# Optimization experiments

Measured on AMD Instinct MI355X. Metric: run time of the kernel, lower is better.

The kernel has to match this reference:

```python
import jax, jax.numpy as jnp
import numpy as np

N = 4096
E = 131072
IN_C, HID, HEADS, OUT_C = 512, 64, 8, 256
BETA = 0.5
NEG_SLOPE = 0.2


def _glorot(key, shape, fan_in, fan_out):
    lim = float(np.sqrt(6.0 / (fan_in + fan_out)))
    return jax.random.uniform(key, shape, jnp.float32, -lim, lim)


def setup_inputs() -> dict:
    key = jax.random.key(0)
    ks = jax.random.split(key, 12)
    x = jax.random.normal(ks[0], (N, IN_C), jnp.float32)
    src = jax.random.randint(ks[1], (E,), 0, N)
    dst = jax.random.randint(ks[2], (E,), 0, N)
    dst = jnp.where(src == dst, (dst + 1) % N, dst)  # no self loops (module removes then re-adds)
    edge_index = jnp.stack([src, dst]).astype(jnp.int64)
    # layer 1: in=512 -> heads=8, out=64 (concat -> 512), residual=False
    W1 = _glorot(ks[3], (IN_C, HEADS * HID), IN_C, HEADS * HID)
    as1 = _glorot(ks[4], (HEADS, HID), HID, HID)
    ad1 = _glorot(ks[5], (HEADS, HID), HID, HID)
    b1 = jnp.zeros((HEADS * HID,), jnp.float32)
    # layer 2: in=512 -> heads=1, out=256, concat=False, residual=True (res_linear needed)
    W2 = _glorot(ks[6], (HEADS * HID, OUT_C), HEADS * HID, OUT_C)
    as2 = _glorot(ks[7], (1, OUT_C), OUT_C, OUT_C)
    ad2 = _glorot(ks[8], (1, OUT_C), OUT_C, OUT_C)
    b2 = jnp.zeros((OUT_C,), jnp.float32)
    resW2 = _glorot(ks[9], (HEADS * HID, OUT_C), HEADS * HID, OUT_C)
    return {"x": x, "edge_index": edge_index, "W1": W1, "as1": as1, "ad1": ad1,
            "b1": b1, "W2": W2, "as2": as2, "ad2": ad2, "b2": b2, "resW2": resW2}


def _seg_softmax(e, seg, n):
    # numerically-stable softmax over edges grouped by destination node
    m = jax.ops.segment_max(e, seg, num_segments=n)  # [n, H]
    a = jnp.exp(e - m[seg])
    s = jax.ops.segment_sum(a, seg, num_segments=n)
    return a / (s[seg] + 1e-16)


def _motif_gat_layer(x, edge_index, W, a_src, a_dst, bias, res_W, heads, out_ch, concat):
    n = x.shape[0]
    residual = x
    h = (x @ W).reshape(n, heads, out_ch)
    # add self loops (input edge_index has none)
    loops = jnp.arange(n, dtype=edge_index.dtype)
    src = jnp.concatenate([edge_index[0], loops])
    dst = jnp.concatenate([edge_index[1], loops])
    xj = h[src]  # [E', H, C]
    xi = h[dst]
    e = (xj * a_src[None]).sum(-1) + (xi * a_dst[None]).sum(-1)  # [E', H]
    alpha_first = _seg_softmax(jax.nn.leaky_relu(e, NEG_SLOPE), dst, n)
    # motif adjacency: dense A^3, row-normalized by clamped row sum
    adj = jnp.zeros((n, n), x.dtype).at[src, dst].set(1.0)
    m3 = adj @ adj @ adj
    m3 = m3 / jnp.clip(m3.sum(-1, keepdims=True), 1.0)
    mw = m3[src, dst][:, None]  # [E', 1]
    alpha_motif = _seg_softmax(jax.nn.leaky_relu(e * mw, NEG_SLOPE), dst, n)
    alpha = BETA * alpha_first + (1.0 - BETA) * alpha_motif  # dropout: eval mode -> identity
    out = jax.ops.segment_sum(alpha[:, :, None] * xj, dst, num_segments=n)  # [n, H, C]
    out = out.reshape(n, heads * out_ch) if concat else out.mean(1)
    if res_W is not None:
        out = out + residual @ res_W
    return out + bias


def reference(x, edge_index, W1, as1, ad1, b1, W2, as2, ad2, b2, resW2):
    h = _motif_gat_layer(x, edge_index, W1, as1, ad1, b1, None, HEADS, HID, True)
    h = jax.nn.elu(h)  # dropout: eval mode -> identity
    out = _motif_gat_layer(h, edge_index, W2, as2, ad2, b2, resW2, 1, OUT_C, False)
    return out
```

## Files before the change

kernel.cpp:

```cpp
#include <hip/hip_runtime.h>
#include <hip/hip_bf16.h>
#include <math.h>

#define NN 4096
#define EE 131072
#define EP (EE + NN)
#define C1 512
#define H1 8
#define C2 256
#define NWORDS 128
#define KP 520

typedef __attribute__((ext_vector_type(8))) short bf16x8;
typedef __attribute__((ext_vector_type(4))) float f32x4;

__device__ __forceinline__ float wredMaxf(float v){
#pragma unroll
  for(int o=32;o;o>>=1) v = fmaxf(v, __shfl_xor(v,o));
  return v;
}
__device__ __forceinline__ float wredSumf(float v){
#pragma unroll
  for(int o=32;o;o>>=1) v += __shfl_xor(v,o);
  return v;
}
__device__ __forceinline__ int wredSumi(int v){
#pragma unroll
  for(int o=32;o;o>>=1) v += __shfl_xor(v,o);
  return v;
}

__device__ __forceinline__ void bfsplit(float v, unsigned short& h, unsigned short& l){
  unsigned bits = __float_as_uint(v);
  h = (unsigned short)(bits>>16);
  float hf = __uint_as_float(bits & 0xFFFF0000u);
  float lo = v - hf;
  l = (unsigned short)(__float_as_uint(lo)>>16);
}

__global__ __launch_bounds__(256) void k_detect(const int* __restrict__ ei32, int* __restrict__ mode){
  __shared__ int any;
  if(threadIdx.x==0) any = 0;
  __syncthreads();
  int nz = 0;
  for(int i=threadIdx.x;i<2048;i+=256) nz |= (ei32[2*i+1] != 0);
  if(nz) atomicOr(&any, 1);
  __syncthreads();
  if(threadIdx.x==0) *mode = any;
}

__device__ __forceinline__ void edge_sd(const int* ei32, int mode, int e, int& s, int& d){
  if(e < EE){
    if(mode==0){ s = ei32[2*e]; d = ei32[2*(EE+e)]; }
    else       { s = ei32[e];   d = ei32[EE+e]; }
  } else { s = e - EE; d = s; }
}

__global__ __launch_bounds__(256) void k_build(const int* __restrict__ ei32, const int* __restrict__ mode,
    unsigned* __restrict__ rowbits, unsigned* __restrict__ colbits, unsigned* __restrict__ cnt){
  int e = blockIdx.x*256 + threadIdx.x;
  if(e >= EP) return;
  int m = *mode, s, d;
  edge_sd(ei32, m, e, s, d);
  atomicOr(&rowbits[s*NWORDS + (d>>5)], 1u<<(d&31));
  atomicOr(&colbits[d*NWORDS + (s>>5)], 1u<<(s&31));
  atomicAdd(&cnt[d], 1u);
}

__global__ __launch_bounds__(256) void k_scan(const unsigned* __restrict__ cnt, unsigned* __restrict__ rowptr){
  __shared__ unsigned part[256];
  int t = threadIdx.x;
  unsigned loc[16]; unsigned s = 0;
#pragma unroll
  for(int i=0;i<16;i++){ loc[i]=cnt[t*16+i]; s+=loc[i]; }
  part[t]=s; __syncthreads();
  for(int off=1;off<256;off<<=1){
    unsigned v = (t>=off)? part[t-off] : 0u;
    __syncthreads();
    part[t]+=v;
    __syncthreads();
  }
  unsigned run = (t==0)? 0u : part[t-1];
#pragma unroll
  for(int i=0;i<16;i++){ rowptr[t*16+i]=run; run+=loc[i]; }
  if(t==255) rowptr[NN]=run;
}

__global__ __launch_bounds__(256) void k_fill(const int* __restrict__ ei32, const int* __restrict__ mode,
    const unsigned* __restrict__ rowptr, unsigned* __restrict__ fill,
    unsigned* __restrict__ csr_src){
  int e = blockIdx.x*256 + threadIdx.x;
  if(e >= EP) return;
  int m = *mode, s, d;
  edge_sd(ei32, m, e, s, d);
  unsigned pos = rowptr[d] + atomicAdd(&fill[d], 1u);
  csr_src[pos]=(unsigned)s;
}

__global__ __launch_bounds__(256) void k_deg(const unsigned* __restrict__ rowbits, float* __restrict__ v1){
  int node = blockIdx.x*4 + (threadIdx.x>>6);
  int lane = threadIdx.x & 63;
  unsigned w0 = rowbits[node*NWORDS + 2*lane];
  unsigned w1 = rowbits[node*NWORDS + 2*lane + 1];
  int c = __popc(w0) + __popc(w1);
  c = wredSumi(c);
  if(lane==0) v1[node] = (float)c;
}

__global__ __launch_bounds__(256) void k_mv(const unsigned* __restrict__ rowbits,
    const float* __restrict__ vin, float* __restrict__ vout){
  int node = blockIdx.x*4 + (threadIdx.x>>6);
  int lane = threadIdx.x & 63;
  float sum = 0.f;
  unsigned w = rowbits[node*NWORDS + 2*lane]; int b0 = lane*64;
  while(w){ int b=__ffs(w)-1; sum += vin[b0+b]; w &= w-1; }
  w = rowbits[node*NWORDS + 2*lane + 1]; b0 = lane*64 + 32;
  while(w){ int b=__ffs(w)-1; sum += vin[b0+b]; w &= w-1; }
  sum = wredSumf(sum);
  if(lane==0) vout[node] = sum;
}

__global__ __launch_bounds__(64) void k_motif(const unsigned* __restrict__ rowbits, const unsigned* __restrict__ colbits,
    const unsigned* __restrict__ rowptr, const unsigned* __restrict__ csr_src,
    const float* __restrict__ v3, float* __restrict__ mwc){
  int d = blockIdx.x;
  int lane = threadIdx.x;
  __shared__ unsigned short nbr[1024];
  __shared__ int cntL;
  if(lane==0) cntL=0;
  __syncthreads();
  {
    unsigned w = colbits[d*NWORDS + 2*lane]; int b0 = lane*64;
    while(w){ int b=__ffs(w)-1; int pos=atomicAdd(&cntL,1); nbr[pos]=(unsigned short)(b0+b); w&=w-1; }
    w = colbits[d*NWORDS + 2*lane + 1]; b0 = lane*64 + 32;
    while(w){ int b=__ffs(w)-1; int pos=atomicAdd(&cntL,1); nbr[pos]=(unsigned short)(b0+b); w&=w-1; }
  }
  __syncthreads();
  int m = cntL;
  unsigned gp[8][2];
#pragma unroll
  for(int p=0;p<8;p++){ gp[p][0]=0u; gp[p][1]=0u; }
  for(int t0=0;t0<m;t0+=4){
    unsigned xa[4], xb[4];
#pragma unroll
    for(int j=0;j<4;j++){
      int tt=t0+j;
      if(tt<m){ int l = nbr[tt]; xa[j]=colbits[l*NWORDS+2*lane]; xb[j]=colbits[l*NWORDS+2*lane+1]; }
      else    { xa[j]=0u; xb[j]=0u; }
    }
#pragma unroll
    for(int j=0;j<4;j++){
      unsigned c = xa[j];
#pragma unroll
      for(int p=0;p<8;p++){ unsigned cy = gp[p][0] & c; gp[p][0] ^= c; c = cy; }
      c = xb[j];
#pragma unroll
      for(int p=0;p<8;p++){ unsigned cy = gp[p][1] & c; gp[p][1] ^= c; c = cy; }
    }
  }
  unsigned base = rowptr[d], deg = rowptr[d+1]-base;
  for(unsigned i0=0;i0<deg;i0+=4){
    unsigned sidx[4], ra[4], rb[4];
#pragma unroll
    for(int j=0;j<4;j++){
      unsigned ii = (i0+j < deg) ? (i0+j) : (deg-1);
      sidx[j] = csr_src[base+ii];
    }
#pragma unroll
    for(int j=0;j<4;j++){ ra[j]=rowbits[sidx[j]*NWORDS+2*lane]; rb[j]=rowbits[sidx[j]*NWORDS+2*lane+1]; }
    int sum[4];
#pragma unroll
    for(int j=0;j<4;j++){
      int s=0;
#pragma unroll
      for(int p=0;p<8;p++)
        s += (__popc(ra[j]&gp[p][0]) + __popc(rb[j]&gp[p][1])) << p;
      sum[j]=s;
    }
    int pk0 = sum[0] | (sum[1]<<16);
    int pk1 = sum[2] | (sum[3]<<16);
    pk0 = wredSumi(pk0); pk1 = wredSumi(pk1);
    if(lane==0){
      int ss[4] = { pk0 & 0xFFFF, (pk0>>16)&0xFFFF, pk1 & 0xFFFF, (pk1>>16)&0xFFFF };
#pragma unroll
      for(int j=0;j<4;j++){
        unsigned idx = i0+j;
        if(idx<deg)
          mwc[base+idx] = (float)ss[j] / fmaxf(v3[csr_src[base+idx]], 1.0f);
      }
    }
  }
}

__global__ __launch_bounds__(256) void k_cvtA(const float* __restrict__ X,
    unsigned short* __restrict__ xh, unsigned short* __restrict__ xl){
  int e = blockIdx.x*256 + threadIdx.x;
  int row = e >> 6;
  int c0 = (e & 63) * 8;
  const float4 v0 = *(const float4*)&X[(size_t)row*C1 + c0];
  const float4 v1 = *(const float4*)&X[(size_t)row*C1 + c0 + 4];
  float vv[8] = {v0.x,v0.y,v0.z,v0.w,v1.x,v1.y,v1.z,v1.w};
  unsigned short h[8], l[8];
#pragma unroll
  for(int j=0;j<8;j++) bfsplit(vv[j], h[j], l[j]);
  *(bf16x8*)&xh[(size_t)row*KP + c0] = *(bf16x8*)h;
  *(bf16x8*)&xl[(size_t)row*KP + c0] = *(bf16x8*)l;
}

__global__ __launch_bounds__(256) void k_cvtB(const float* __restrict__ W, int N,
    unsigned short* __restrict__ bh, unsigned short* __restrict__ bl){
  int n = blockIdx.x; int t = threadIdx.x;
  int k = t*2;
  float a = W[(size_t)k*N + n];
  float b = W[(size_t)(k+1)*N + n];
  unsigned short h0,l0,h1,l1;
  bfsplit(a,h0,l0); bfsplit(b,h1,l1);
  unsigned short hp[2]={h0,h1}, lp[2]={l0,l1};
  *(unsigned int*)&bh[(size_t)n*KP + k] = *(unsigned int*)hp;
  *(unsigned int*)&bl[(size_t)n*KP + k] = *(unsigned int*)lp;
}

__global__ __launch_bounds__(256) void k_gemm_mfma(
    const unsigned short* __restrict__ Ah, const unsigned short* __restrict__ Al,
    const unsigned short* __restrict__ Bh, const unsigned short* __restrict__ Bl,
    float* __restrict__ C, int M, int N){
  __shared__ unsigned short Ahs[64][40], Als[64][40], Bhs[64][40], Bls[64][40];
  int bm = blockIdx.y*64, bn = blockIdx.x*64;
  int t = threadIdx.x, lane = t&63, w = t>>6;
  int wm = (w>>1)*32, wn = (w&1)*32;
  f32x4 acc[2][2];
#pragma unroll
  for(int i=0;i<2;i++)
#pragma unroll
    for(int j=0;j<2;j++) acc[i][j] = (f32x4){0.f,0.f,0.f,0.f};
  int sm = t>>2, skq = (t&3)*8;
  const unsigned short* pAh = &Ah[(size_t)(bm+sm)*KP + skq];
  const unsigned short* pAl = &Al[(size_t)(bm+sm)*KP + skq];
  const unsigned short* pBh = &Bh[(size_t)(bn+sm)*KP + skq];
  const unsigned short* pBl = &Bl[(size_t)(bn+sm)*KP + skq];
  int fr = lane&15, kg = lane>>4;
  for(int k0=0;k0<C1;k0+=32){
    *(bf16x8*)&Ahs[sm][skq] = *(const bf16x8*)(pAh + k0);
    *(bf16x8*)&Als[sm][skq] = *(const bf16x8*)(pAl + k0);
    *(bf16x8*)&Bhs[sm][skq] = *(const bf16x8*)(pBh + k0);
    *(bf16x8*)&Bls[sm][skq] = *(const bf16x8*)(pBl + k0);
    __syncthreads();
    bf16x8 ah[2], al[2], bh[2], bl[2];
#pragma unroll
    for(int i=0;i<2;i++){
      ah[i] = *(bf16x8*)&Ahs[wm + i*16 + fr][kg*8];
      al[i] = *(bf16x8*)&Als[wm + i*16 + fr][kg*8];
      bh[i] = *(bf16x8*)&Bhs[wn + i*16 + fr][kg*8];
      bl[i] = *(bf16x8*)&Bls[wn + i*16 + fr][kg*8];
    }
#pragma unroll
    for(int i=0;i<2;i++)
#pragma unroll
      for(int j=0;j<2;j++){
        acc[i][j] = __builtin_amdgcn_mfma_f32_16x16x32_bf16(ah[i], bh[j], acc[i][j], 0,0,0);
        acc[i][j] = __builtin_amdgcn_mfma_f32_16x16x32_bf16(ah[i], bl[j], acc[i][j], 0,0,0);
        acc[i][j] = __builtin_amdgcn_mfma_f32_16x16x32_bf16(al[i], bh[j], acc[i][j], 0,0,0);
      }
    __syncthreads();
  }
#pragma unroll
  for(int i=0;i<2;i++)
#pragma unroll
    for(int j=0;j<2;j++){
      int gr = bm + wm + i*16 + kg*4;
      int gc = bn + wn + j*16 + fr;
#pragma unroll
      for(int e=0;e<4;e++)
        C[(size_t)(gr+e)*N + gc] = acc[i][j][e];
    }
}

__global__ __launch_bounds__(512) void k_attn1(const float* __restrict__ hpre, const float* __restrict__ as1,
    const float* __restrict__ ad1, float* __restrict__ asrc, float* __restrict__ adst){
  int n = blockIdx.x; int t = threadIdx.x; int lane = t&63; int h = t>>6;
  float v = hpre[n*C1 + t];
  float p1 = v*as1[t], p2 = v*ad1[t];
  p1 = wredSumf(p1); p2 = wredSumf(p2);
  if(lane==0){ asrc[n*H1+h]=p1; adst[n*H1+h]=p2; }
}

__global__ __launch_bounds__(128) void k_layer1(const unsigned* __restrict__ rowptr, const unsigned* __restrict__ csr_src,
    const float* __restrict__ mwc, const float* __restrict__ asrc, const float* __restrict__ adst,
    const float* __restrict__ hpre, const float* __restrict__ b1,
    unsigned short* __restrict__ h1h, unsigned short* __restrict__ h1l){
  int n = blockIdx.x;
  int tid = threadIdx.x, lane = tid&63, wv = tid>>6;
  unsigned base = rowptr[n], deg = rowptr[n+1]-base;
  __shared__ float a1s[128][9];
  __shared__ float a2s[128][9];
  __shared__ unsigned ssrc[128];
  __shared__ float red1[2][8], red2[2][8];
  __shared__ float snm1[8], snm2[8], sscl1[8], sscl2[8];
  __shared__ float sS1[8], sS2[8], sM1[8], sM2[8];
  __shared__ float adsts[8];
  if(tid<8){ adsts[tid]=adst[n*H1+tid]; sM1[tid]=-3.0e38f; sM2[tid]=-3.0e38f; sS1[tid]=0.f; sS2[tid]=0.f; }
  __syncthreads();
  int h = tid>>4;
  float4 acc1={0.f,0.f,0.f,0.f}, acc2={0.f,0.f,0.f,0.f};
  for(unsigned c0=0;c0<deg;c0+=128){
    int csz = (int)min(128u, deg-c0);
    bool act = (tid < csz);
    float el[8], em[8];
    if(act){
      unsigned s = csr_src[base+c0+tid];
      ssrc[tid]=s;
      float mwv = mwc[base+c0+tid];
      const float4 a0v = *(const float4*)&asrc[s*H1];
      const float4 a1v = *(const float4*)&asrc[s*H1+4];
      float as8[8]={a0v.x,a0v.y,a0v.z,a0v.w,a1v.x,a1v.y,a1v.z,a1v.w};
#pragma unroll
      for(int hh=0;hh<8;hh++){
        float ev = as8[hh]+adsts[hh];
        el[hh] = ev>=0.f? ev : 0.2f*ev;
        float evm = ev*mwv;
        em[hh] = evm>=0.f? evm : 0.2f*evm;
      }
    } else {
#pragma unroll
      for(int hh=0;hh<8;hh++){ el[hh]=-3.0e38f; em[hh]=-3.0e38f; }
    }
    float mx1[8], mx2[8];
#pragma unroll
    for(int hh=0;hh<8;hh++){ mx1[hh]=wredMaxf(el[hh]); mx2[hh]=wredMaxf(em[hh]); }
    if(lane==0){
#pragma unroll
      for(int hh=0;hh<8;hh++){ red1[wv][hh]=mx1[hh]; red2[wv][hh]=mx2[hh]; }
    }
    __syncthreads();
    if(tid<8){
      float cm1 = fmaxf(red1[0][tid], red1[1][tid]);
      float cm2 = fmaxf(red2[0][tid], red2[1][tid]);
      float nm1 = fmaxf(sM1[tid], cm1), nm2 = fmaxf(sM2[tid], cm2);
      sscl1[tid] = expf(sM1[tid]-nm1); sscl2[tid] = expf(sM2[tid]-nm2);
      snm1[tid]=nm1; snm2[tid]=nm2;
      sM1[tid]=nm1;  sM2[tid]=nm2;
    }
    __syncthreads();
    float s1l[8], s2l[8];
#pragma unroll
    for(int hh=0;hh<8;hh++){
      float a1v = act? expf(el[hh]-snm1[hh]) : 0.f;
      float a2v = act? expf(em[hh]-snm2[hh]) : 0.f;
      if(act){ a1s[tid][hh]=a1v; a2s[tid][hh]=a2v; }
      s1l[hh]=a1v; s2l[hh]=a2v;
    }
#pragma unroll
    for(int hh=0;hh<8;hh++){ s1l[hh]=wredSumf(s1l[hh]); s2l[hh]=wredSumf(s2l[hh]); }
    if(lane==0){
#pragma unroll
      for(int hh=0;hh<8;hh++){ red1[wv][hh]=s1l[hh]; red2[wv][hh]=s2l[hh]; }
    }
    __syncthreads();
    if(tid<8){
      sS1[tid] = sS1[tid]*sscl1[tid] + red1[0][tid]+red1[1][tid];
      sS2[tid] = sS2[tid]*sscl2[tid] + red2[0][tid]+red2[1][tid];
    }
    {
      float sc1 = sscl1[h], sc2 = sscl2[h];
      acc1.x*=sc1; acc1.y*=sc1; acc1.z*=sc1; acc1.w*=sc1;
      acc2.x*=sc2; acc2.y*=sc2; acc2.z*=sc2; acc2.w*=sc2;
    }
    for(int i0=0;i0<csz;i0+=4){
      int jn = min(4, csz-i0);
      unsigned sj[4]; float a1j[4], a2j[4];
#pragma unroll
      for(int j=0;j<4;j++){
        int ii = (j<jn)? i0+j : i0;
        sj[j]=ssrc[ii]; a1j[j]=a1s[ii][h]; a2j[j]=a2s[ii][h];
      }
      float4 hv[4];
#pragma unroll
      for(int j=0;j<4;j++) hv[j] = *(const float4*)&hpre[(size_t)sj[j]*C1 + tid*4];
#pragma unroll
      for(int j=0;j<4;j++){
        float w1 = (j<jn)? a1j[j] : 0.f;
        float w2 = (j<jn)? a2j[j] : 0.f;
        acc1.x += w1*hv[j].x; acc1.y += w1*hv[j].y; acc1.z += w1*hv[j].z; acc1.w += w1*hv[j].w;
        acc2.x += w2*hv[j].x; acc2.y += w2*hv[j].y; acc2.z += w2*hv[j].z; acc2.w += w2*hv[j].w;
      }
    }
    __syncthreads();
  }
  float r1 = 0.5f/(sS1[h]+1e-16f), r2 = 0.5f/(sS2[h]+1e-16f);
  int cc = tid*4;
  const float4 bv = *(const float4*)&b1[cc];
  float o[4];
  float vx = acc1.x*r1 + acc2.x*r2 + bv.x; o[0] = vx>0.f? vx : expm1f(vx);
  float vy = acc1.y*r1 + acc2.y*r2 + bv.y; o[1] = vy>0.f? vy : expm1f(vy);
  float vz = acc1.z*r1 + acc2.z*r2 + bv.z; o[2] = vz>0.f? vz : expm1f(vz);
  float vw = acc1.w*r1 + acc2.w*r2 + bv.w; o[3] = vw>0.f? vw : expm1f(vw);
  unsigned short hh4[4], ll4[4];
#pragma unroll
  for(int j=0;j<4;j++) bfsplit(o[j], hh4[j], ll4[j]);
  *(ushort4*)&h1h[(size_t)n*KP + cc] = *(ushort4*)hh4;
  *(ushort4*)&h1l[(size_t)n*KP + cc] = *(ushort4*)ll4;
}

__global__ __launch_bounds__(64) void k_attn2(const float* __restrict__ h2, const float* __restrict__ as2,
    const float* __restrict__ ad2, float* __restrict__ asrc, float* __restrict__ adst){
  int n = blockIdx.x; int lane = threadIdx.x;
  const float4 hv = *(const float4*)&h2[(size_t)n*512 + lane*4];
  const float4 av = *(const float4*)&as2[lane*4];
  const float4 dv = *(const float4*)&ad2[lane*4];
  float p1 = hv.x*av.x + hv.y*av.y + hv.z*av.z + hv.w*av.w;
  float p2 = hv.x*dv.x + hv.y*dv.y + hv.z*dv.z + hv.w*dv.w;
  p1 = wredSumf(p1); p2 = wredSumf(p2);
  if(lane==0){ asrc[n]=p1; adst[n]=p2; }
}

__global__ __launch_bounds__(64) void k_layer2(const unsigned* __restrict__ rowptr, const unsigned* __restrict__ csr_src,
    const float* __restrict__ mwc, const float* __restrict__ asrc, const float* __restrict__ adst,
    const float* __restrict__ h2, const float* __restrict__ res,
    const float* __restrict__ b2, float* __restrict__ out){
  int n = blockIdx.x; int lane = threadIdx.x;
  unsigned base = rowptr[n], deg = rowptr[n+1]-base;
  __shared__ float a1s[64], a2s[64];
  __shared__ unsigned ssrc[64];
  float ad = adst[n];
  float M1=-3.0e38f, M2=-3.0e38f, S1=0.f, S2=0.f;
  float4 acc1={0.f,0.f,0.f,0.f}, acc2={0.f,0.f,0.f,0.f};
  for(unsigned c0=0;c0<deg;c0+=64){
    int csz = (int)min(64u, deg-c0);
    bool act = (lane < csz);
    float el=-3.0e38f, em=-3.0e38f;
    if(act){
      unsigned s = csr_src[base+c0+lane];
      ssrc[lane]=s;
      float mwv = mwc[base+c0+lane];
      float ev = asrc[s] + ad;
      el = ev>=0.f? ev : 0.2f*ev;
      float evm = ev*mwv;
      em = evm>=0.f? evm : 0.2f*evm;
    }
    float nm1 = fmaxf(M1, wredMaxf(el));
    float nm2 = fmaxf(M2, wredMaxf(em));
    float sc1 = expf(M1-nm1), sc2 = expf(M2-nm2);
    M1=nm1; M2=nm2;
    float a1 = act? expf(el-nm1) : 0.f;
    float a2 = act? expf(em-nm2) : 0.f;
    if(act){ a1s[lane]=a1; a2s[lane]=a2; }
    S1 = S1*sc1 + wredSumf(a1);
    S2 = S2*sc2 + wredSumf(a2);
    acc1.x*=sc1; acc1.y*=sc1; acc1.z*=sc1; acc1.w*=sc1;
    acc2.x*=sc2; acc2.y*=sc2; acc2.z*=sc2; acc2.w*=sc2;
    __syncthreads();
    for(int i0=0;i0<csz;i0+=4){
      int jn = min(4, csz-i0);
      unsigned sj[4]; float a1j[4], a2j[4];
#pragma unroll
      for(int j=0;j<4;j++){
        int ii = (j<jn)? i0+j : i0;
        sj[j]=ssrc[ii]; a1j[j]=a1s[ii]; a2j[j]=a2s[ii];
      }
      float4 hv[4];
#pragma unroll
      for(int j=0;j<4;j++) hv[j] = *(const float4*)&h2[(size_t)sj[j]*512 + lane*4];
#pragma unroll
      for(int j=0;j<4;j++){
        float w1 = (j<jn)? a1j[j] : 0.f;
        float w2 = (j<jn)? a2j[j] : 0.f;
        acc1.x += w1*hv[j].x; acc1.y += w1*hv[j].y; acc1.z += w1*hv[j].z; acc1.w += w1*hv[j].w;
        acc2.x += w2*hv[j].x; acc2.y += w2*hv[j].y; acc2.z += w2*hv[j].z; acc2.w += w2*hv[j].w;
      }
    }
    __syncthreads();
  }
  float r1 = 0.5f/(S1+1e-16f), r2 = 0.5f/(S2+1e-16f);
  int cc = lane*4;
  const float4 rv = *(const float4*)&res[(size_t)n*512 + cc];
  const float4 bv = *(const float4*)&b2[cc];
  float4 o = {acc1.x*r1 + acc2.x*r2 + rv.x + bv.x,
              acc1.y*r1 + acc2.y*r2 + rv.y + bv.y,
              acc1.z*r1 + acc2.z*r2 + rv.z + bv.z,
              acc1.w*r1 + acc2.w*r2 + rv.w + bv.w};
  *(float4*)&out[(size_t)n*C2 + cc] = o;
}

extern "C" void kernel_launch(void* const* d_in, const int* in_sizes, int n_in,
                              void* d_out, int out_size, void* d_ws, size_t ws_size,
                              hipStream_t stream) {
  const float* x    = (const float*)d_in[0];
  const int*   ei32 = (const int*)d_in[1];
  const float* W1   = (const float*)d_in[2];
  const float* as1  = (const float*)d_in[3];
  const float* ad1  = (const float*)d_in[4];
  const float* b1   = (const float*)d_in[5];
  const float* W2   = (const float*)d_in[6];
  const float* as2  = (const float*)d_in[7];
  const float* ad2  = (const float*)d_in[8];
  const float* b2   = (const float*)d_in[9];
  const float* resW2= (const float*)d_in[10];
  float* out = (float*)d_out;

  char* p = (char*)d_ws;
  auto alloc = [&](size_t b){ void* r=(void*)p; p += (b + 255) & ~(size_t)255; return r; };
  unsigned* rowbits = (unsigned*)alloc((size_t)NN*NWORDS*4);
  unsigned* colbits = (unsigned*)alloc((size_t)NN*NWORDS*4);
  unsigned* cnt     = (unsigned*)alloc(NN*4);
  unsigned* fill    = (unsigned*)alloc(NN*4);
  unsigned* rowptr  = (unsigned*)alloc((NN+4)*4);
  float* v1 = (float*)alloc(NN*4);
  float* v2 = (float*)alloc(NN*4);
  float* v3 = (float*)alloc(NN*4);
  unsigned* csr_src = (unsigned*)alloc((size_t)EP*4);
  float* mwc  = (float*)alloc((size_t)EP*4);
  float* asrc1= (float*)alloc(NN*H1*4);
  float* adst1= (float*)alloc(NN*H1*4);
  unsigned short* xsh = (unsigned short*)alloc((size_t)NN*KP*2);
  unsigned short* xsl = (unsigned short*)alloc((size_t)NN*KP*2);
  unsigned short* bt1h= (unsigned short*)alloc((size_t)C1*KP*2);
  unsigned short* bt1l= (unsigned short*)alloc((size_t)C1*KP*2);
  unsigned short* bt2h= (unsigned short*)alloc((size_t)C1*KP*2);
  unsigned short* bt2l= (unsigned short*)alloc((size_t)C1*KP*2);
  float* hpre = (float*)alloc((size_t)NN*C1*4);
  unsigned short* h1h = (unsigned short*)alloc((size_t)NN*KP*2);
  unsigned short* h1l = (unsigned short*)alloc((size_t)NN*KP*2);
  float* c23  = (float*)alloc((size_t)NN*512*4);
  float* asrc2= (float*)alloc(NN*4);
  float* adst2= (float*)alloc(NN*4);
  int* mode   = (int*)alloc(256);
  float* h2  = c23;
  float* res = c23 + 256;

  hipMemsetAsync(rowbits, 0, (size_t)NN*NWORDS*4*2, stream);
  hipMemsetAsync(cnt, 0, (size_t)NN*4*2, stream);

  k_detect<<<1,256,0,stream>>>(ei32, mode);
  k_build<<<(EP+255)/256,256,0,stream>>>(ei32, mode, rowbits, colbits, cnt);
  k_scan<<<1,256,0,stream>>>(cnt, rowptr);
  k_fill<<<(EP+255)/256,256,0,stream>>>(ei32, mode, rowptr, fill, csr_src);
  k_deg<<<NN/4,256,0,stream>>>(rowbits, v1);
  k_mv<<<NN/4,256,0,stream>>>(rowbits, v1, v2);
  k_mv<<<NN/4,256,0,stream>>>(rowbits, v2, v3);
  k_motif<<<NN,64,0,stream>>>(rowbits, colbits, rowptr, csr_src, v3, mwc);

  k_cvtA<<<(NN*64)/256,256,0,stream>>>(x, xsh, xsl);
  k_cvtB<<<C1,256,0,stream>>>(W1, C1, bt1h, bt1l);
  k_cvtB<<<C2,256,0,stream>>>(W2, C2, bt2h, bt2l);
  k_cvtB<<<C2,256,0,stream>>>(resW2, C2, bt2h + (size_t)C2*KP, bt2l + (size_t)C2*KP);

  k_gemm_mfma<<<dim3(C1/64, NN/64),256,0,stream>>>(xsh, xsl, bt1h, bt1l, hpre, NN, C1);
  k_attn1<<<NN,512,0,stream>>>(hpre, as1, ad1, asrc1, adst1);
  k_layer1<<<NN,128,0,stream>>>(rowptr, csr_src, mwc, asrc1, adst1, hpre, b1, h1h, h1l);

  k_gemm_mfma<<<dim3(512/64, NN/64),256,0,stream>>>(h1h, h1l, bt2h, bt2l, c23, NN, 512);
  k_attn2<<<NN,64,0,stream>>>(h2, as2, ad2, asrc2, adst2);
  k_layer2<<<NN,64,0,stream>>>(rowptr, csr_src, mwc, asrc2, adst2, h2, res, b2, out);
}
```

Baseline: 267.7 us.

## Fold mode detection into build kernels, merge launches, pipeline GEMM, widen gathers

Drops the separate mode-detection kernel and has each edge kernel infer int32/int64 layout from the first few words. The two memsets become one, and the three weight-conversion launches become one kernel, cutting launch count. The MFMA GEMM now uses a K tile of 64 with register prefetch of the next tile, so global loads overlap compute, and the layer aggregation loops gather 8 neighbour rows per batch instead of 4. The detection heuristic samples only 8 words and could misclassify unusual inputs, and the larger batches raise register pressure.

```diff
diff --git a/kernel.cpp b/kernel.cpp
--- a/kernel.cpp
+++ b/kernel.cpp
@@ -38,15 +38,11 @@
   l = (unsigned short)(__float_as_uint(lo)>>16);
 }
 
-__global__ __launch_bounds__(256) void k_detect(const int* __restrict__ ei32, int* __restrict__ mode){
-  __shared__ int any;
-  if(threadIdx.x==0) any = 0;
-  __syncthreads();
-  int nz = 0;
-  for(int i=threadIdx.x;i<2048;i+=256) nz |= (ei32[2*i+1] != 0);
-  if(nz) atomicOr(&any, 1);
-  __syncthreads();
-  if(threadIdx.x==0) *mode = any;
+__device__ __forceinline__ int detect_mode(const int* __restrict__ ei32){
+  unsigned nz = 0;
+#pragma unroll
+  for(int i=1;i<16;i+=2) nz |= (unsigned)ei32[i];
+  return nz != 0;
 }
 
 __device__ __forceinline__ void edge_sd(const int* ei32, int mode, int e, int& s, int& d){
@@ -56,11 +52,11 @@
   } else { s = e - EE; d = s; }
 }
 
-__global__ __launch_bounds__(256) void k_build(const int* __restrict__ ei32, const int* __restrict__ mode,
+__global__ __launch_bounds__(256) void k_build(const int* __restrict__ ei32,
     unsigned* __restrict__ rowbits, unsigned* __restrict__ colbits, unsigned* __restrict__ cnt){
   int e = blockIdx.x*256 + threadIdx.x;
   if(e >= EP) return;
-  int m = *mode, s, d;
+  int m = detect_mode(ei32), s, d;
   edge_sd(ei32, m, e, s, d);
   atomicOr(&rowbits[s*NWORDS + (d>>5)], 1u<<(d&31));
   atomicOr(&colbits[d*NWORDS + (s>>5)], 1u<<(s&31));
@@ -86,12 +82,12 @@
   if(t==255) rowptr[NN]=run;
 }
 
-__global__ __launch_bounds__(256) void k_fill(const int* __restrict__ ei32, const int* __restrict__ mode,
+__global__ __launch_bounds__(256) void k_fill(const int* __restrict__ ei32,
     const unsigned* __restrict__ rowptr, unsigned* __restrict__ fill,
     unsigned* __restrict__ csr_src){
   int e = blockIdx.x*256 + threadIdx.x;
   if(e >= EP) return;
-  int m = *mode, s, d;
+  int m = detect_mode(ei32), s, d;
   edge_sd(ei32, m, e, s, d);
   unsigned pos = rowptr[d] + atomicAdd(&fill[d], 1u);
   csr_src[pos]=(unsigned)s;
@@ -207,24 +203,30 @@
   *(bf16x8*)&xl[(size_t)row*KP + c0] = *(bf16x8*)l;
 }
 
-__global__ __launch_bounds__(256) void k_cvtB(const float* __restrict__ W, int N,
-    unsigned short* __restrict__ bh, unsigned short* __restrict__ bl){
-  int n = blockIdx.x; int t = threadIdx.x;
+__global__ __launch_bounds__(256) void k_cvtB_all(const float* __restrict__ W1f,
+    const float* __restrict__ W2f, const float* __restrict__ Wrf,
+    unsigned short* __restrict__ b1h, unsigned short* __restrict__ b1l,
+    unsigned short* __restrict__ b2h, unsigned short* __restrict__ b2l){
+  int blk = blockIdx.x; int t = threadIdx.x;
+  const float* W; int N, n, nrow; unsigned short *bh, *bl;
+  if(blk < 512){ W=W1f; N=512; n=blk;     nrow=n;     bh=b1h; bl=b1l; }
+  else if(blk < 768){ W=W2f; N=256; n=blk-512; nrow=n;     bh=b2h; bl=b2l; }
+  else { W=Wrf; N=256; n=blk-768; nrow=n+256; bh=b2h; bl=b2l; }
   int k = t*2;
   float a = W[(size_t)k*N + n];
   float b = W[(size_t)(k+1)*N + n];
   unsigned short h0,l0,h1,l1;
   bfsplit(a,h0,l0); bfsplit(b,h1,l1);
   unsigned short hp[2]={h0,h1}, lp[2]={l0,l1};
-  *(unsigned int*)&bh[(size_t)n*KP + k] = *(unsigned int*)hp;
-  *(unsigned int*)&bl[(size_t)n*KP + k] = *(unsigned int*)lp;
+  *(unsigned int*)&bh[(size_t)nrow*KP + k] = *(unsigned int*)hp;
+  *(unsigned int*)&bl[(size_t)nrow*KP + k] = *(unsigned int*)lp;
 }
 
 __global__ __launch_bounds__(256) void k_gemm_mfma(
     const unsigned short* __restrict__ Ah, const unsigned short* __restrict__ Al,
     const unsigned short* __restrict__ Bh, const unsigned short* __restrict__ Bl,
     float* __restrict__ C, int M, int N){
-  __shared__ unsigned short Ahs[64][40], Als[64][40], Bhs[64][40], Bls[64][40];
+  __shared__ unsigned short Ahs[64][72], Als[64][72], Bhs[64][72], Bls[64][72];
   int bm = blockIdx.y*64, bn = blockIdx.x*64;
   int t = threadIdx.x, lane = t&63, w = t>>6;
   int wm = (w>>1)*32, wn = (w&1)*32;
@@ -233,34 +235,55 @@
   for(int i=0;i<2;i++)
 #pragma unroll
     for(int j=0;j<2;j++) acc[i][j] = (f32x4){0.f,0.f,0.f,0.f};
-  int sm = t>>2, skq = (t&3)*8;
-  const unsigned short* pAh = &Ah[(size_t)(bm+sm)*KP + skq];
-  const unsigned short* pAl = &Al[(size_t)(bm+sm)*KP + skq];
-  const unsigned short* pBh = &Bh[(size_t)(bn+sm)*KP + skq];
-  const unsigned short* pBl = &Bl[(size_t)(bn+sm)*KP + skq];
+  int sm = t>>2, sk = (t&3)*16;
+  const unsigned short* pAh = &Ah[(size_t)(bm+sm)*KP + sk];
+  const unsigned short* pAl = &Al[(size_t)(bm+sm)*KP + sk];
+  const unsigned short* pBh = &Bh[(size_t)(bn+sm)*KP + sk];
+  const unsigned short* pBl = &Bl[(size_t)(bn+sm)*KP + sk];
   int fr = lane&15, kg = lane>>4;
-  for(int k0=0;k0<C1;k0+=32){
-    *(bf16x8*)&Ahs[sm][skq] = *(const bf16x8*)(pAh + k0);
-    *(bf16x8*)&Als[sm][skq] = *(const bf16x8*)(pAl + k0);
-    *(bf16x8*)&Bhs[sm][skq] = *(const bf16x8*)(pBh + k0);
-    *(bf16x8*)&Bls[sm][skq] = *(const bf16x8*)(pBl + k0);
-    __syncthreads();
-    bf16x8 ah[2], al[2], bh[2], bl[2];
-#pragma unroll
-    for(int i=0;i<2;i++){
-      ah[i] = *(bf16x8*)&Ahs[wm + i*16 + fr][kg*8];
-      al[i] = *(bf16x8*)&Als[wm + i*16 + fr][kg*8];
-      bh[i] = *(bf16x8*)&Bhs[wn + i*16 + fr][kg*8];
-      bl[i] = *(bf16x8*)&Bls[wn + i*16 + fr][kg*8];
-    }
-#pragma unroll
-    for(int i=0;i<2;i++)
-#pragma unroll
-      for(int j=0;j<2;j++){
-        acc[i][j] = __builtin_amdgcn_mfma_f32_16x16x32_bf16(ah[i], bh[j], acc[i][j], 0,0,0);
-        acc[i][j] = __builtin_amdgcn_mfma_f32_16x16x32_bf16(ah[i], bl[j], acc[i][j], 0,0,0);
-        acc[i][j] = __builtin_amdgcn_mfma_f32_16x16x32_bf16(al[i], bh[j], acc[i][j], 0,0,0);
-      }
+  bf16x8 rah0 = *(const bf16x8*)(pAh), rah1 = *(const bf16x8*)(pAh+8);
+  bf16x8 ral0 = *(const bf16x8*)(pAl), ral1 = *(const bf16x8*)(pAl+8);
+  bf16x8 rbh0 = *(const bf16x8*)(pBh), rbh1 = *(const bf16x8*)(pBh+8);
+  bf16x8 rbl0 = *(const bf16x8*)(pBl), rbl1 = *(const bf16x8*)(pBl+8);
+  *(bf16x8*)&Ahs[sm][sk] = rah0; *(bf16x8*)&Ahs[sm][sk+8] = rah1;
+  *(bf16x8*)&Als[sm][sk] = ral0; *(bf16x8*)&Als[sm][sk+8] = ral1;
+  *(bf16x8*)&Bhs[sm][sk] = rbh0; *(bf16x8*)&Bhs[sm][sk+8] = rbh1;
+  *(bf16x8*)&Bls[sm][sk] = rbl0; *(bf16x8*)&Bls[sm][sk+8] = rbl1;
+  __syncthreads();
+  for(int k0=0;k0<C1;k0+=64){
+    int kn = k0+64;
+    if(kn<C1){
+      rah0 = *(const bf16x8*)(pAh+kn); rah1 = *(const bf16x8*)(pAh+kn+8);
+      ral0 = *(const bf16x8*)(pAl+kn); ral1 = *(const bf16x8*)(pAl+kn+8);
+      rbh0 = *(const bf16x8*)(pBh+kn); rbh1 = *(const bf16x8*)(pBh+kn+8);
+      rbl0 = *(const bf16x8*)(pBl+kn); rbl1 = *(const bf16x8*)(pBl+kn+8);
+    }
+#pragma unroll
+    for(int ks=0;ks<64;ks+=32){
+      bf16x8 fah[2], fal[2], fbh[2], fbl[2];
+#pragma unroll
+      for(int i=0;i<2;i++){
+        fah[i] = *(bf16x8*)&Ahs[wm + i*16 + fr][ks + kg*8];
+        fal[i] = *(bf16x8*)&Als[wm + i*16 + fr][ks + kg*8];
+        fbh[i] = *(bf16x8*)&Bhs[wn + i*16 + fr][ks + kg*8];
+        fbl[i] = *(bf16x8*)&Bls[wn + i*16 + fr][ks + kg*8];
+      }
+#pragma unroll
+      for(int i=0;i<2;i++)
+#pragma unroll
+        for(int j=0;j<2;j++){
+          acc[i][j] = __builtin_amdgcn_mfma_f32_16x16x32_bf16(fah[i], fbh[j], acc[i][j], 0,0,0);
+          acc[i][j] = __builtin_amdgcn_mfma_f32_16x16x32_bf16(fah[i], fbl[j], acc[i][j], 0,0,0);
+          acc[i][j] = __builtin_amdgcn_mfma_f32_16x16x32_bf16(fal[i], fbh[j], acc[i][j], 0,0,0);
+        }
+    }
+    __syncthreads();
+    if(kn<C1){
+      *(bf16x8*)&Ahs[sm][sk] = rah0; *(bf16x8*)&Ahs[sm][sk+8] = rah1;
+      *(bf16x8*)&Als[sm][sk] = ral0; *(bf16x8*)&Als[sm][sk+8] = ral1;
+      *(bf16x8*)&Bhs[sm][sk] = rbh0; *(bf16x8*)&Bhs[sm][sk+8] = rbh1;
+      *(bf16x8*)&Bls[sm][sk] = rbl0; *(bf16x8*)&Bls[sm][sk+8] = rbl1;
+    }
     __syncthreads();
   }
 #pragma unroll
@@ -365,19 +388,19 @@
       acc1.x*=sc1; acc1.y*=sc1; acc1.z*=sc1; acc1.w*=sc1;
       acc2.x*=sc2; acc2.y*=sc2; acc2.z*=sc2; acc2.w*=sc2;
     }
-    for(int i0=0;i0<csz;i0+=4){
-      int jn = min(4, csz-i0);
-      unsigned sj[4]; float a1j[4], a2j[4];
-#pragma unroll
-      for(int j=0;j<4;j++){
+    for(int i0=0;i0<csz;i0+=8){
+      int jn = min(8, csz-i0);
+      unsigned sj[8]; float a1j[8], a2j[8];
+#pragma unroll
+      for(int j=0;j<8;j++){
         int ii = (j<jn)? i0+j : i0;
         sj[j]=ssrc[ii]; a1j[j]=a1s[ii][h]; a2j[j]=a2s[ii][h];
       }
-      float4 hv[4];
-#pragma unroll
-      for(int j=0;j<4;j++) hv[j] = *(const float4*)&hpre[(size_t)sj[j]*C1 + tid*4];
-#pragma unroll
-      for(int j=0;j<4;j++){
+      float4 hv[8];
+#pragma unroll
+      for(int j=0;j<8;j++) hv[j] = *(const float4*)&hpre[(size_t)sj[j]*C1 + tid*4];
+#pragma unroll
+      for(int j=0;j<8;j++){
         float w1 = (j<jn)? a1j[j] : 0.f;
         float w2 = (j<jn)? a2j[j] : 0.f;
         acc1.x += w1*hv[j].x; acc1.y += w1*hv[j].y; acc1.z += w1*hv[j].z; acc1.w += w1*hv[j].w;
@@ -449,19 +472,19 @@
     acc1.x*=sc1; acc1.y*=sc1; acc1.z*=sc1; acc1.w*=sc1;
     acc2.x*=sc2; acc2.y*=sc2; acc2.z*=sc2; acc2.w*=sc2;
     __syncthreads();
-    for(int i0=0;i0<csz;i0+=4){
-      int jn = min(4, csz-i0);
-      unsigned sj[4]; float a1j[4], a2j[4];
-#pragma unroll
-      for(int j=0;j<4;j++){
+    for(int i0=0;i0<csz;i0+=8){
+      int jn = min(8, csz-i0);
+      unsigned sj[8]; float a1j[8], a2j[8];
+#pragma unroll
+      for(int j=0;j<8;j++){
         int ii = (j<jn)? i0+j : i0;
         sj[j]=ssrc[ii]; a1j[j]=a1s[ii]; a2j[j]=a2s[ii];
       }
-      float4 hv[4];
-#pragma unroll
-      for(int j=0;j<4;j++) hv[j] = *(const float4*)&h2[(size_t)sj[j]*512 + lane*4];
-#pragma unroll
-      for(int j=0;j<4;j++){
+      float4 hv[8];
+#pragma unroll
+      for(int j=0;j<8;j++) hv[j] = *(const float4*)&h2[(size_t)sj[j]*512 + lane*4];
+#pragma unroll
+      for(int j=0;j<8;j++){
         float w1 = (j<jn)? a1j[j] : 0.f;
         float w2 = (j<jn)? a2j[j] : 0.f;
         acc1.x += w1*hv[j].x; acc1.y += w1*hv[j].y; acc1.z += w1*hv[j].z; acc1.w += w1*hv[j].w;
@@ -503,6 +526,7 @@
   unsigned* colbits = (unsigned*)alloc((size_t)NN*NWORDS*4);
   unsigned* cnt     = (unsigned*)alloc(NN*4);
   unsigned* fill    = (unsigned*)alloc(NN*4);
+  size_t zbytes = (size_t)NN*NWORDS*4*2 + (size_t)NN*4*2;
   unsigned* rowptr  = (unsigned*)alloc((NN+4)*4);
   float* v1 = (float*)alloc(NN*4);
   float* v2 = (float*)alloc(NN*4);
@@ -523,26 +547,21 @@
   float* c23  = (float*)alloc((size_t)NN*512*4);
   float* asrc2= (float*)alloc(NN*4);
   float* adst2= (float*)alloc(NN*4);
-  int* mode   = (int*)alloc(256);
   float* h2  = c23;
   float* res = c23 + 256;
 
-  hipMemsetAsync(rowbits, 0, (size_t)NN*NWORDS*4*2, stream);
-  hipMemsetAsync(cnt, 0, (size_t)NN*4*2, stream);
-
-  k_detect<<<1,256,0,stream>>>(ei32, mode);
-  k_build<<<(EP+255)/256,256,0,stream>>>(ei32, mode, rowbits, colbits, cnt);
+  hipMemsetAsync(rowbits, 0, zbytes, stream);
+
+  k_build<<<(EP+255)/256,256,0,stream>>>(ei32, rowbits, colbits, cnt);
   k_scan<<<1,256,0,stream>>>(cnt, rowptr);
-  k_fill<<<(EP+255)/256,256,0,stream>>>(ei32, mode, rowptr, fill, csr_src);
+  k_fill<<<(EP+255)/256,256,0,stream>>>(ei32, rowptr, fill, csr_src);
   k_deg<<<NN/4,256,0,stream>>>(rowbits, v1);
   k_mv<<<NN/4,256,0,stream>>>(rowbits, v1, v2);
   k_mv<<<NN/4,256,0,stream>>>(rowbits, v2, v3);
   k_motif<<<NN,64,0,stream>>>(rowbits, colbits, rowptr, csr_src, v3, mwc);
 
   k_cvtA<<<(NN*64)/256,256,0,stream>>>(x, xsh, xsl);
-  k_cvtB<<<C1,256,0,stream>>>(W1, C1, bt1h, bt1l);
-  k_cvtB<<<C2,256,0,stream>>>(W2, C2, bt2h, bt2l);
-  k_cvtB<<<C2,256,0,stream>>>(resW2, C2, bt2h + (size_t)C2*KP, bt2l + (size_t)C2*KP);
+  k_cvtB_all<<<1024,256,0,stream>>>(W1, W2, resW2, bt1h, bt1l, bt2h, bt2l);
 
   k_gemm_mfma<<<dim3(C1/64, NN/64),256,0,stream>>>(xsh, xsl, bt1h, bt1l, hpre, NN, C1);
   k_attn1<<<NN,512,0,stream>>>(hpre, as1, ad1, asrc1, adst1);
```

Result: faster. 253.6 us (-5.3%).
